# Optimization experiments

Measured on AMD Instinct MI355X. Metric: run time of the kernel, lower is better.

The kernel has to match this reference:

```python
import jax, jax.numpy as jnp
import numpy as np

N_NODES = 100000
N_EDGES = 1600000
IN_FEATS, HID, NUM_CLS = 128, 128, 40


def setup_inputs() -> dict:
    key = jax.random.key(0)
    ks = jax.random.split(key, 5)
    x = jax.random.normal(ks[0], (N_NODES, IN_FEATS), dtype=jnp.float32)
    # xavier-like scale for weights
    W1 = jax.random.normal(ks[1], (IN_FEATS, HID), dtype=jnp.float32) * (1.0 / np.sqrt(IN_FEATS))
    b1 = jnp.zeros((HID,), dtype=jnp.float32)
    W2 = jax.random.normal(ks[2], (HID, NUM_CLS), dtype=jnp.float32) * (1.0 / np.sqrt(HID))
    b2 = jnp.zeros((NUM_CLS,), dtype=jnp.float32)
    src = jax.random.randint(ks[3], (N_EDGES,), 0, N_NODES, dtype=jnp.int32)
    dst = jax.random.randint(ks[4], (N_EDGES,), 0, N_NODES, dtype=jnp.int32)
    return {"x": x, "W1": W1, "b1": b1, "W2": W2, "b2": b2, "src": src, "dst": dst}


def _graph_conv(h, W, b, src, dst, src_norm, dst_norm, n_nodes):
    # DGL GraphConv, norm='both': D_out^{-1/2} A D_in^{-1/2} H W + b
    # (weight-first vs aggregate-first ordering in DGL is mathematically identical)
    hs = h * src_norm[:, None]                      # [N, d] source-side norm
    msg = hs[src]                                   # [E, d] gather
    agg = jax.ops.segment_sum(msg, dst, num_segments=n_nodes)  # [N, d] scatter-add
    agg = agg * dst_norm[:, None]                   # dest-side norm
    return agg @ W + b


def reference(x, W1, b1, W2, b2, src, dst):
    n = x.shape[0]
    ones = jnp.ones(src.shape[0], dtype=x.dtype)
    out_deg = jnp.clip(jax.ops.segment_sum(ones, src, num_segments=n), 1.0)
    in_deg = jnp.clip(jax.ops.segment_sum(ones, dst, num_segments=n), 1.0)
    src_norm = out_deg ** -0.5
    dst_norm = in_deg ** -0.5
    h = jax.nn.relu(_graph_conv(x, W1, b1, src, dst, src_norm, dst_norm, n))
    return _graph_conv(h, W2, b2, src, dst, src_norm, dst_norm, n)
```

## Files before the change

kernel.cpp:

```cpp
#include <hip/hip_runtime.h>

constexpr int NN   = 100000;
constexpr int NE   = 1600000;
constexpr int INF  = 128;
constexpr int NC   = 40;

constexpr int BKSH = 9;
constexpr int NBK  = (NN + 511) / 512;
constexpr int EPB  = 4096;
constexpr int PBLK = (NE + EPB - 1) / EPB;
constexpr int CAP  = 14336;
constexpr int HB   = 391;

typedef __attribute__((ext_vector_type(8))) short short8;
typedef __attribute__((ext_vector_type(4))) float f32x4;

__device__ __forceinline__ float bflo(unsigned int u) { return __uint_as_float(u << 16); }
__device__ __forceinline__ float bfhi(unsigned int u) { return __uint_as_float(u & 0xffff0000u); }
__device__ __forceinline__ unsigned short f2bf(float f) {
    unsigned int u = __float_as_uint(f);
    return (unsigned short)((u + 0x7fffu + ((u >> 16) & 1u)) >> 16);
}
__device__ __forceinline__ unsigned int pack2(float a, float b) {
    return (unsigned int)f2bf(a) | ((unsigned int)f2bf(b) << 16);
}

__global__ __launch_bounds__(256) void histconv_kernel(const int* __restrict__ src,
                                                       const int* __restrict__ dst,
                                                       unsigned int* __restrict__ bcntD,
                                                       unsigned int* __restrict__ bcntS,
                                                       const float* __restrict__ x,
                                                       const float* __restrict__ W1,
                                                       const float* __restrict__ W2,
                                                       unsigned short* __restrict__ xh,
                                                       unsigned short* __restrict__ w1t,
                                                       unsigned short* __restrict__ w2t) {
    const int b = blockIdx.x;
    const int tid = threadIdx.x;
    if (b < HB) {
        __shared__ unsigned int hcD[NBK];
        __shared__ unsigned int hcS[NBK];
        for (int i = tid; i < NBK; i += 256) { hcD[i] = 0u; hcS[i] = 0u; }
        __syncthreads();
        int gid = b * 256 + tid;
        int stride = HB * 256;
        for (int e = gid; e < NE; e += stride) {
            atomicAdd(&hcD[dst[e] >> BKSH], 1u);
            atomicAdd(&hcS[src[e] >> BKSH], 1u);
        }
        __syncthreads();
        for (int i = tid; i < NBK; i += 256) {
            if (hcD[i]) atomicAdd(&bcntD[i], hcD[i]);
            if (hcS[i]) atomicAdd(&bcntS[i], hcS[i]);
        }
    } else if (b < HB + 6250) {
        int j = (b - HB) * 256 + tid;
        float4 v0 = ((const float4*)x)[2 * j];
        float4 v1 = ((const float4*)x)[2 * j + 1];
        uint4 o;
        o.x = pack2(v0.x, v0.y);
        o.y = pack2(v0.z, v0.w);
        o.z = pack2(v1.x, v1.y);
        o.w = pack2(v1.z, v1.w);
        ((uint4*)xh)[j] = o;
    } else if (b == HB + 6250) {
        for (int i = tid; i < 128 * 128; i += 256) {
            int k = i >> 7, n = i & 127;
            w1t[n * 128 + k] = f2bf(W1[i]);
        }
    } else {
        for (int i = tid; i < 48 * 128; i += 256) {
            int n = i >> 7, k = i & 127;
            w2t[i] = f2bf((n < NC) ? W2[k * NC + n] : 0.f);
        }
    }
}

__global__ __launch_bounds__(256) void partition_kernel(const int* __restrict__ src,
                                                        const int* __restrict__ dst,
                                                        const unsigned int* __restrict__ bcntD,
                                                        const unsigned int* __restrict__ bcntS,
                                                        int* __restrict__ curD_g,
                                                        int* __restrict__ curS_g,
                                                        int* __restrict__ epartsD,
                                                        unsigned short* __restrict__ epartsS) {
    __shared__ int sc[256];
    __shared__ int cntD[NBK], gadjD[NBK], curD[NBK];
    __shared__ int cntS[NBK], gadjS[NBK], curS[NBK];
    __shared__ int baselD[NBK], baselS[NBK];
    __shared__ int stageD[EPB];
    __shared__ unsigned short stageS[EPB];
    __shared__ unsigned char bidD[EPB];
    __shared__ unsigned char bidS[EPB];
    const int tid = threadIdx.x;
    const int e0 = blockIdx.x * EPB;
    const int total = min(EPB, NE - e0);

    {
        int v = (tid < NBK) ? (int)bcntD[tid] : 0;
        sc[tid] = v;
        __syncthreads();
        for (int off = 1; off < 256; off <<= 1) {
            int t = (tid >= off) ? sc[tid - off] : 0;
            __syncthreads();
            sc[tid] += t;
            __syncthreads();
        }
        if (tid < NBK) baselD[tid] = sc[tid] - v;
        __syncthreads();
        v = (tid < NBK) ? (int)bcntS[tid] : 0;
        sc[tid] = v;
        __syncthreads();
        for (int off = 1; off < 256; off <<= 1) {
            int t = (tid >= off) ? sc[tid - off] : 0;
            __syncthreads();
            sc[tid] += t;
            __syncthreads();
        }
        if (tid < NBK) baselS[tid] = sc[tid] - v;
    }
    for (int i = tid; i < NBK; i += 256) { cntD[i] = 0; cntS[i] = 0; }
    __syncthreads();
    for (int i = tid; i < total; i += 256) {
        atomicAdd(&cntD[dst[e0 + i] >> BKSH], 1);
        atomicAdd(&cntS[src[e0 + i] >> BKSH], 1);
    }
    __syncthreads();
    {
        int v = (tid < NBK) ? cntD[tid] : 0;
        sc[tid] = v;
        __syncthreads();
        for (int off = 1; off < 256; off <<= 1) {
            int t = (tid >= off) ? sc[tid - off] : 0;
            __syncthreads();
            sc[tid] += t;
            __syncthreads();
        }
        if (tid < NBK) {
            int excl = sc[tid] - v;
            curD[tid] = excl;
            int g = (v > 0) ? atomicAdd(&curD_g[tid], v) : 0;
            gadjD[tid] = baselD[tid] + g - excl;
        }
        __syncthreads();
        v = (tid < NBK) ? cntS[tid] : 0;
        sc[tid] = v;
        __syncthreads();
        for (int off = 1; off < 256; off <<= 1) {
            int t = (tid >= off) ? sc[tid - off] : 0;
            __syncthreads();
            sc[tid] += t;
            __syncthreads();
        }
        if (tid < NBK) {
            int excl = sc[tid] - v;
            curS[tid] = excl;
            int g = (v > 0) ? atomicAdd(&curS_g[tid], v) : 0;
            gadjS[tid] = baselS[tid] + g - excl;
        }
    }
    __syncthreads();
    for (int i = tid; i < total; i += 256) {
        int s = src[e0 + i];
        int d = dst[e0 + i];
        int bD = d >> BKSH;
        int offD = atomicAdd(&curD[bD], 1);
        stageD[offD] = s | ((d - (bD << BKSH)) << 17);
        bidD[offD] = (unsigned char)bD;
        int bS = s >> BKSH;
        int offS = atomicAdd(&curS[bS], 1);
        stageS[offS] = (unsigned short)(s - (bS << BKSH));
        bidS[offS] = (unsigned char)bS;
    }
    __syncthreads();
    for (int j = tid; j < total; j += 256) {
        int b = bidD[j];
        epartsD[gadjD[b] + j] = stageD[j];
    }
    for (int j = tid; j < total; j += 256) {
        int b = bidS[j];
        epartsS[gadjS[b] + j] = stageS[j];
    }
}

__global__ __launch_bounds__(512) void pass2_kernel(const int* __restrict__ epartsD,
                                                    const unsigned short* __restrict__ epartsS,
                                                    const unsigned int* __restrict__ bcntD,
                                                    const unsigned int* __restrict__ bcntS,
                                                    int* __restrict__ row_ptr,
                                                    int* __restrict__ esrc,
                                                    float* __restrict__ srcn,
                                                    float* __restrict__ dstn) {
    __shared__ int hist[512];
    __shared__ int cur[512];
    __shared__ int histS[512];
    __shared__ int lesrc[CAP];
    __shared__ int base_s, cnt_s, baseS_s, cntS_s;
    const int tid = threadIdx.x;
    const int b = blockIdx.x;

    {
        int v = (tid < NBK) ? (int)bcntD[tid] : 0;
        hist[tid] = v;
        __syncthreads();
        for (int off = 1; off < 512; off <<= 1) {
            int t = (tid >= off) ? hist[tid - off] : 0;
            __syncthreads();
            hist[tid] += t;
            __syncthreads();
        }
        if (tid == b) { base_s = hist[b] - v; cnt_s = v; }
        __syncthreads();
        v = (tid < NBK) ? (int)bcntS[tid] : 0;
        hist[tid] = v;
        __syncthreads();
        for (int off = 1; off < 512; off <<= 1) {
            int t = (tid >= off) ? hist[tid - off] : 0;
            __syncthreads();
            hist[tid] += t;
            __syncthreads();
        }
        if (tid == b) { baseS_s = hist[b] - v; cntS_s = v; }
        __syncthreads();
    }
    const int base = base_s;
    const int cnt = cnt_s;
    const int baseS = baseS_s;
    const int cntS = cntS_s;
    const int n0 = b << BKSH;
    const int nloc = min(512, NN - n0);

    hist[tid] = 0;
    histS[tid] = 0;
    __syncthreads();
    for (int j = tid; j < cnt; j += 512)
        atomicAdd(&hist[epartsD[base + j] >> 17], 1);
    for (int j = tid; j < cntS; j += 512)
        atomicAdd(&histS[(int)epartsS[baseS + j]], 1);
    __syncthreads();
    int myc = hist[tid];
    int mycS = histS[tid];
    for (int off = 1; off < 512; off <<= 1) {
        int t = (tid >= off) ? hist[tid - off] : 0;
        __syncthreads();
        hist[tid] += t;
        __syncthreads();
    }
    int excl = hist[tid] - myc;
    cur[tid] = excl;
    if (tid < nloc) {
        int g = n0 + tid;
        row_ptr[g] = base + excl;
        dstn[g] = rsqrtf(fmaxf((float)myc, 1.0f));
        srcn[g] = rsqrtf(fmaxf((float)mycS, 1.0f));
    }
    if (b == NBK - 1 && tid == 0) row_ptr[NN] = NE;
    __syncthreads();
    if (cnt <= CAP) {
        for (int j = tid; j < cnt; j += 512) {
            int rec = epartsD[base + j];
            int pos = atomicAdd(&cur[rec >> 17], 1);
            lesrc[pos] = rec & 0x1FFFF;
        }
        __syncthreads();
        for (int j = tid; j < cnt; j += 512) esrc[base + j] = lesrc[j];
    } else {
        for (int j = tid; j < cnt; j += 512) {
            int rec = epartsD[base + j];
            int pos = atomicAdd(&cur[rec >> 17], 1);
            esrc[base + pos] = rec & 0x1FFFF;
        }
    }
}

__global__ __launch_bounds__(256) void fused_kernel(const int* __restrict__ row_ptr,
                                                    const int* __restrict__ esrc,
                                                    const unsigned short* __restrict__ xh,
                                                    const float* __restrict__ srcn,
                                                    const unsigned short* __restrict__ w1t,
                                                    const unsigned short* __restrict__ w2t,
                                                    const float* __restrict__ b1,
                                                    const float* __restrict__ dstn,
                                                    unsigned short* __restrict__ hwb) {
    __shared__ unsigned short At[64 * 128];
    __shared__ float dn[64], sn[64], b1l[128];
    const int tid  = threadIdx.x;
    const int r0   = blockIdx.x * 64;
    const int wv   = tid >> 6;
    const int lane = tid & 63;

    if (tid < 64) {
        int r = r0 + tid;
        dn[tid] = (r < NN) ? dstn[r] : 0.f;
        sn[tid] = (r < NN) ? srcn[r] : 0.f;
    }
    if (tid >= 64 && tid < 192) b1l[tid - 64] = b1[tid - 64];
    __syncthreads();

    const int quad = lane >> 4;
    const int l16  = lane & 15;
    for (int i = 0; i < 16; ++i) {
        const int node = r0 + wv * 16 + i;
        float a0 = 0.f, a1 = 0.f, a2 = 0.f, a3 = 0.f;
        float a4 = 0.f, a5 = 0.f, a6 = 0.f, a7 = 0.f;
        if (node < NN) {
            int beg = __builtin_amdgcn_readfirstlane(row_ptr[node]);
            int end = __builtin_amdgcn_readfirstlane(row_ptr[node + 1]);
            for (int e = beg; e < end; e += 24) {
                const int rem = end - e;
                int s[6];
#pragma unroll
                for (int t = 0; t < 6; ++t) {
                    int slot = t * 4 + quad;
                    s[t] = esrc[(slot < rem) ? (e + slot) : beg];
                }
                float n[6];
                uint4 u[6];
#pragma unroll
                for (int t = 0; t < 6; ++t) {
                    int slot = t * 4 + quad;
                    n[t] = (slot < rem) ? srcn[s[t]] : 0.f;
                    u[t] = ((const uint4*)(xh + (size_t)s[t] * INF))[l16];
                }
#pragma unroll
                for (int t = 0; t < 6; ++t) {
                    a0 += bflo(u[t].x) * n[t];
                    a1 += bfhi(u[t].x) * n[t];
                    a2 += bflo(u[t].y) * n[t];
                    a3 += bfhi(u[t].y) * n[t];
                    a4 += bflo(u[t].z) * n[t];
                    a5 += bfhi(u[t].z) * n[t];
                    a6 += bflo(u[t].w) * n[t];
                    a7 += bfhi(u[t].w) * n[t];
                }
            }
        }
        a0 += __shfl_down(a0, 32); a1 += __shfl_down(a1, 32);
        a2 += __shfl_down(a2, 32); a3 += __shfl_down(a3, 32);
        a4 += __shfl_down(a4, 32); a5 += __shfl_down(a5, 32);
        a6 += __shfl_down(a6, 32); a7 += __shfl_down(a7, 32);
        a0 += __shfl_down(a0, 16); a1 += __shfl_down(a1, 16);
        a2 += __shfl_down(a2, 16); a3 += __shfl_down(a3, 16);
        a4 += __shfl_down(a4, 16); a5 += __shfl_down(a5, 16);
        a6 += __shfl_down(a6, 16); a7 += __shfl_down(a7, 16);
        if (lane < 16) {
            uint4 o;
            o.x = pack2(a0, a1);
            o.y = pack2(a2, a3);
            o.z = pack2(a4, a5);
            o.w = pack2(a6, a7);
            *(uint4*)&At[(wv * 16 + i) * 128 + l16 * 8] = o;
        }
    }

    const int lrow  = lane & 15;
    const int lquad = lane >> 4;

    short8 afrag[4];
#pragma unroll
    for (int ks = 0; ks < 4; ++ks)
        afrag[ks] = *(const short8*)&At[(wv * 16 + lrow) * 128 + ks * 32 + lquad * 8];
    float hreg[8][4];
#pragma unroll
    for (int nt = 0; nt < 8; ++nt) {
        f32x4 acc = {0.f, 0.f, 0.f, 0.f};
#pragma unroll
        for (int ks = 0; ks < 4; ++ks) {
            short8 bfr = *(const short8*)&w1t[(nt * 16 + lrow) * 128 + ks * 32 + lquad * 8];
            acc = __builtin_amdgcn_mfma_f32_16x16x32_bf16(afrag[ks], bfr, acc, 0, 0, 0);
        }
#pragma unroll
        for (int i = 0; i < 4; ++i) hreg[nt][i] = acc[i];
    }
#pragma unroll
    for (int nt = 0; nt < 8; ++nt) {
        int col = nt * 16 + lrow;
        float bb = b1l[col];
#pragma unroll
        for (int i = 0; i < 4; ++i) {
            int row = wv * 16 + lquad * 4 + i;
            At[row * 128 + col] = f2bf(fmaxf(hreg[nt][i] * dn[row] + bb, 0.f));
        }
    }

#pragma unroll
    for (int ks = 0; ks < 4; ++ks)
        afrag[ks] = *(const short8*)&At[(wv * 16 + lrow) * 128 + ks * 32 + lquad * 8];
#pragma unroll
    for (int nt = 0; nt < 3; ++nt) {
        f32x4 acc = {0.f, 0.f, 0.f, 0.f};
#pragma unroll
        for (int ks = 0; ks < 4; ++ks) {
            short8 bfr = *(const short8*)&w2t[(nt * 16 + lrow) * 128 + ks * 32 + lquad * 8];
            acc = __builtin_amdgcn_mfma_f32_16x16x32_bf16(afrag[ks], bfr, acc, 0, 0, 0);
        }
        int col = nt * 16 + lrow;
        if (col < NC) {
#pragma unroll
            for (int i = 0; i < 4; ++i) {
                int row = wv * 16 + lquad * 4 + i;
                int grow = r0 + row;
                if (grow < NN)
                    hwb[(size_t)grow * NC + col] = f2bf(acc[i] * sn[row]);
            }
        }
    }
}

__global__ __launch_bounds__(256) void gather2_kernel(const int* __restrict__ row_ptr,
                                                      const int* __restrict__ esrc,
                                                      const unsigned short* __restrict__ hwb,
                                                      const float* __restrict__ dst_norm,
                                                      const float* __restrict__ b2,
                                                      float* __restrict__ out) {
    int node = (blockIdx.x * blockDim.x + threadIdx.x) >> 6;
    int lane = threadIdx.x & 63;
    if (node >= NN) return;
    int beg = __builtin_amdgcn_readfirstlane(row_ptr[node]);
    int end = __builtin_amdgcn_readfirstlane(row_ptr[node + 1]);
    const int g = lane / 10;
    const int j = lane - g * 10;
    const bool active = (g < 6);
    float4 acc = make_float4(0.f, 0.f, 0.f, 0.f);
    for (int e = beg; e < end; e += 18) {
        const int rem = end - e;
        int s[3];
        float m[3];
#pragma unroll
        for (int q = 0; q < 3; ++q) {
            int slot = q * 6 + g;
            bool v = active && (slot < rem);
            int idx = v ? (e + slot) : beg;
            s[q] = esrc[idx];
            m[q] = v ? 1.f : 0.f;
        }
        uint2 u[3];
#pragma unroll
        for (int q = 0; q < 3; ++q)
            u[q] = ((const uint2*)(hwb + (size_t)s[q] * NC))[j];
#pragma unroll
        for (int q = 0; q < 3; ++q) {
            acc.x += bflo(u[q].x) * m[q];
            acc.y += bfhi(u[q].x) * m[q];
            acc.z += bflo(u[q].y) * m[q];
            acc.w += bfhi(u[q].y) * m[q];
        }
    }
    float4 tot = acc;
#pragma unroll
    for (int k = 1; k < 6; ++k) {
        tot.x += __shfl(acc.x, j + 10 * k);
        tot.y += __shfl(acc.y, j + 10 * k);
        tot.z += __shfl(acc.z, j + 10 * k);
        tot.w += __shfl(acc.w, j + 10 * k);
    }
    if (lane < 10) {
        float dnv = dst_norm[node];
        float4 bb = ((const float4*)b2)[j];
        float4 o;
        o.x = tot.x * dnv + bb.x;
        o.y = tot.y * dnv + bb.y;
        o.z = tot.z * dnv + bb.z;
        o.w = tot.w * dnv + bb.w;
        ((float4*)(out + (size_t)node * NC))[j] = o;
    }
}

extern "C" void kernel_launch(void* const* d_in, const int* in_sizes, int n_in,
                              void* d_out, int out_size, void* d_ws, size_t ws_size,
                              hipStream_t stream) {
    const float* x   = (const float*)d_in[0];
    const float* W1  = (const float*)d_in[1];
    const float* b1  = (const float*)d_in[2];
    const float* W2  = (const float*)d_in[3];
    const float* b2  = (const float*)d_in[4];
    const int*   src = (const int*)d_in[5];
    const int*   dst = (const int*)d_in[6];
    float* out = (float*)d_out;

    float* srcn = (float*)d_ws;
    unsigned int* bcntD = (unsigned int*)(srcn + NN);
    unsigned int* bcntS = bcntD + 256;
    int* curD = (int*)(bcntS + 256);
    int* curS = curD + 256;
    int* row_ptr = curS + 256;
    float* dstn  = (float*)(row_ptr + NN + 1);
    int* esrc    = (int*)(dstn + NN);
    size_t ofs = (size_t)NN + 1024 + (NN + 1) + NN + NE;
    ofs = (ofs + 3) & ~(size_t)3;
    unsigned short* xh   = (unsigned short*)((float*)d_ws + ofs);
    unsigned short* w1t  = xh + (size_t)NN * INF;
    unsigned short* w2t  = w1t + 128 * 128;
    unsigned short* hwb  = w2t + 48 * 128;

    int* epartsD = (int*)d_out;
    unsigned short* epartsS = (unsigned short*)(epartsD + NE);

    hipMemsetAsync(bcntD, 0, 1024 * sizeof(int), stream);

    histconv_kernel<<<HB + 6252, 256, 0, stream>>>(src, dst, bcntD, bcntS,
                                                   x, W1, W2, xh, w1t, w2t);
    partition_kernel<<<PBLK, 256, 0, stream>>>(src, dst, bcntD, bcntS, curD, curS,
                                               epartsD, epartsS);
    pass2_kernel<<<NBK, 512, 0, stream>>>(epartsD, epartsS, bcntD, bcntS,
                                          row_ptr, esrc, srcn, dstn);
    fused_kernel<<<(NN + 63) / 64, 256, 0, stream>>>(row_ptr, esrc, xh, srcn,
                                                     w1t, w2t, b1, dstn, hwb);
    gather2_kernel<<<(NN * 64 + 255) / 256, 256, 0, stream>>>(row_ptr, esrc, hwb,
                                                              dstn, b2, out);
}
```

Baseline: 318.7 us.

## Replace two-pass bucket partition CSR build with global-atomic degree count and scatter

Replaces the shared-memory bucketed two-pass partition (partition_kernel plus pass2_kernel) with direct global atomic per-node in/out degree counting in the histogram kernel, a per-bucket scan kernel that writes row_ptr and cursors, and a simple scatter kernel using global atomics on per-node cursors. This cuts the staging traffic through the output buffer and the extra passes over the edge list. In exchange it adds 3.2M random global atomics for degrees and 1.6M contended atomic cursor updates with scattered writes, and edge order within each row becomes nondeterministic, which can change floating-point summation order.

```diff
diff --git a/kernel.cpp b/kernel.cpp
--- a/kernel.cpp
+++ b/kernel.cpp
@@ -7,9 +7,6 @@
 
 constexpr int BKSH = 9;
 constexpr int NBK  = (NN + 511) / 512;
-constexpr int EPB  = 4096;
-constexpr int PBLK = (NE + EPB - 1) / EPB;
-constexpr int CAP  = 14336;
 constexpr int HB   = 391;
 
 typedef __attribute__((ext_vector_type(8))) short short8;
@@ -27,8 +24,9 @@
 
 __global__ __launch_bounds__(256) void histconv_kernel(const int* __restrict__ src,
                                                        const int* __restrict__ dst,
+                                                       int* __restrict__ indeg,
+                                                       int* __restrict__ outdeg,
                                                        unsigned int* __restrict__ bcntD,
-                                                       unsigned int* __restrict__ bcntS,
                                                        const float* __restrict__ x,
                                                        const float* __restrict__ W1,
                                                        const float* __restrict__ W2,
@@ -39,20 +37,20 @@
     const int tid = threadIdx.x;
     if (b < HB) {
         __shared__ unsigned int hcD[NBK];
-        __shared__ unsigned int hcS[NBK];
-        for (int i = tid; i < NBK; i += 256) { hcD[i] = 0u; hcS[i] = 0u; }
+        for (int i = tid; i < NBK; i += 256) hcD[i] = 0u;
         __syncthreads();
         int gid = b * 256 + tid;
         int stride = HB * 256;
         for (int e = gid; e < NE; e += stride) {
-            atomicAdd(&hcD[dst[e] >> BKSH], 1u);
-            atomicAdd(&hcS[src[e] >> BKSH], 1u);
-        }
-        __syncthreads();
-        for (int i = tid; i < NBK; i += 256) {
+            int d = dst[e];
+            int s = src[e];
+            atomicAdd(&indeg[d], 1);
+            atomicAdd(&outdeg[s], 1);
+            atomicAdd(&hcD[d >> BKSH], 1u);
+        }
+        __syncthreads();
+        for (int i = tid; i < NBK; i += 256)
             if (hcD[i]) atomicAdd(&bcntD[i], hcD[i]);
-            if (hcS[i]) atomicAdd(&bcntS[i], hcS[i]);
-        }
     } else if (b < HB + 6250) {
         int j = (b - HB) * 256 + tid;
         float4 v0 = ((const float4*)x)[2 * j];
@@ -76,201 +74,69 @@
     }
 }
 
-__global__ __launch_bounds__(256) void partition_kernel(const int* __restrict__ src,
-                                                        const int* __restrict__ dst,
-                                                        const unsigned int* __restrict__ bcntD,
-                                                        const unsigned int* __restrict__ bcntS,
-                                                        int* __restrict__ curD_g,
-                                                        int* __restrict__ curS_g,
-                                                        int* __restrict__ epartsD,
-                                                        unsigned short* __restrict__ epartsS) {
-    __shared__ int sc[256];
-    __shared__ int cntD[NBK], gadjD[NBK], curD[NBK];
-    __shared__ int cntS[NBK], gadjS[NBK], curS[NBK];
-    __shared__ int baselD[NBK], baselS[NBK];
-    __shared__ int stageD[EPB];
-    __shared__ unsigned short stageS[EPB];
-    __shared__ unsigned char bidD[EPB];
-    __shared__ unsigned char bidS[EPB];
+__global__ __launch_bounds__(512) void scan_kernel(const unsigned int* __restrict__ bcntD,
+                                                   const int* __restrict__ indeg,
+                                                   const int* __restrict__ outdeg,
+                                                   int* __restrict__ row_ptr,
+                                                   int* __restrict__ cur,
+                                                   float* __restrict__ dstn,
+                                                   float* __restrict__ srcn) {
+    __shared__ int sc[512];
+    __shared__ int base_s;
     const int tid = threadIdx.x;
-    const int e0 = blockIdx.x * EPB;
-    const int total = min(EPB, NE - e0);
+    const int b = blockIdx.x;
 
     {
         int v = (tid < NBK) ? (int)bcntD[tid] : 0;
         sc[tid] = v;
         __syncthreads();
-        for (int off = 1; off < 256; off <<= 1) {
+        for (int off = 1; off < 512; off <<= 1) {
             int t = (tid >= off) ? sc[tid - off] : 0;
             __syncthreads();
             sc[tid] += t;
             __syncthreads();
         }
-        if (tid < NBK) baselD[tid] = sc[tid] - v;
-        __syncthreads();
-        v = (tid < NBK) ? (int)bcntS[tid] : 0;
-        sc[tid] = v;
-        __syncthreads();
-        for (int off = 1; off < 256; off <<= 1) {
-            int t = (tid >= off) ? sc[tid - off] : 0;
-            __syncthreads();
-            sc[tid] += t;
-            __syncthreads();
-        }
-        if (tid < NBK) baselS[tid] = sc[tid] - v;
-    }
-    for (int i = tid; i < NBK; i += 256) { cntD[i] = 0; cntS[i] = 0; }
-    __syncthreads();
-    for (int i = tid; i < total; i += 256) {
-        atomicAdd(&cntD[dst[e0 + i] >> BKSH], 1);
-        atomicAdd(&cntS[src[e0 + i] >> BKSH], 1);
-    }
-    __syncthreads();
-    {
-        int v = (tid < NBK) ? cntD[tid] : 0;
-        sc[tid] = v;
-        __syncthreads();
-        for (int off = 1; off < 256; off <<= 1) {
-            int t = (tid >= off) ? sc[tid - off] : 0;
-            __syncthreads();
-            sc[tid] += t;
-            __syncthreads();
-        }
-        if (tid < NBK) {
-            int excl = sc[tid] - v;
-            curD[tid] = excl;
-            int g = (v > 0) ? atomicAdd(&curD_g[tid], v) : 0;
-            gadjD[tid] = baselD[tid] + g - excl;
-        }
-        __syncthreads();
-        v = (tid < NBK) ? cntS[tid] : 0;
-        sc[tid] = v;
-        __syncthreads();
-        for (int off = 1; off < 256; off <<= 1) {
-            int t = (tid >= off) ? sc[tid - off] : 0;
-            __syncthreads();
-            sc[tid] += t;
-            __syncthreads();
-        }
-        if (tid < NBK) {
-            int excl = sc[tid] - v;
-            curS[tid] = excl;
-            int g = (v > 0) ? atomicAdd(&curS_g[tid], v) : 0;
-            gadjS[tid] = baselS[tid] + g - excl;
-        }
-    }
-    __syncthreads();
-    for (int i = tid; i < total; i += 256) {
-        int s = src[e0 + i];
-        int d = dst[e0 + i];
-        int bD = d >> BKSH;
-        int offD = atomicAdd(&curD[bD], 1);
-        stageD[offD] = s | ((d - (bD << BKSH)) << 17);
-        bidD[offD] = (unsigned char)bD;
-        int bS = s >> BKSH;
-        int offS = atomicAdd(&curS[bS], 1);
-        stageS[offS] = (unsigned short)(s - (bS << BKSH));
-        bidS[offS] = (unsigned char)bS;
-    }
-    __syncthreads();
-    for (int j = tid; j < total; j += 256) {
-        int b = bidD[j];
-        epartsD[gadjD[b] + j] = stageD[j];
-    }
-    for (int j = tid; j < total; j += 256) {
-        int b = bidS[j];
-        epartsS[gadjS[b] + j] = stageS[j];
-    }
-}
-
-__global__ __launch_bounds__(512) void pass2_kernel(const int* __restrict__ epartsD,
-                                                    const unsigned short* __restrict__ epartsS,
-                                                    const unsigned int* __restrict__ bcntD,
-                                                    const unsigned int* __restrict__ bcntS,
-                                                    int* __restrict__ row_ptr,
-                                                    int* __restrict__ esrc,
-                                                    float* __restrict__ srcn,
-                                                    float* __restrict__ dstn) {
-    __shared__ int hist[512];
-    __shared__ int cur[512];
-    __shared__ int histS[512];
-    __shared__ int lesrc[CAP];
-    __shared__ int base_s, cnt_s, baseS_s, cntS_s;
-    const int tid = threadIdx.x;
-    const int b = blockIdx.x;
-
-    {
-        int v = (tid < NBK) ? (int)bcntD[tid] : 0;
-        hist[tid] = v;
-        __syncthreads();
-        for (int off = 1; off < 512; off <<= 1) {
-            int t = (tid >= off) ? hist[tid - off] : 0;
-            __syncthreads();
-            hist[tid] += t;
-            __syncthreads();
-        }
-        if (tid == b) { base_s = hist[b] - v; cnt_s = v; }
-        __syncthreads();
-        v = (tid < NBK) ? (int)bcntS[tid] : 0;
-        hist[tid] = v;
-        __syncthreads();
-        for (int off = 1; off < 512; off <<= 1) {
-            int t = (tid >= off) ? hist[tid - off] : 0;
-            __syncthreads();
-            hist[tid] += t;
-            __syncthreads();
-        }
-        if (tid == b) { baseS_s = hist[b] - v; cntS_s = v; }
+        if (tid == b) base_s = sc[b] - v;
         __syncthreads();
     }
     const int base = base_s;
-    const int cnt = cnt_s;
-    const int baseS = baseS_s;
-    const int cntS = cntS_s;
     const int n0 = b << BKSH;
     const int nloc = min(512, NN - n0);
 
-    hist[tid] = 0;
-    histS[tid] = 0;
+    int deg = 0, odeg = 0;
+    if (tid < nloc) {
+        deg = indeg[n0 + tid];
+        odeg = outdeg[n0 + tid];
+    }
+    sc[tid] = deg;
     __syncthreads();
-    for (int j = tid; j < cnt; j += 512)
-        atomicAdd(&hist[epartsD[base + j] >> 17], 1);
-    for (int j = tid; j < cntS; j += 512)
-        atomicAdd(&histS[(int)epartsS[baseS + j]], 1);
-    __syncthreads();
-    int myc = hist[tid];
-    int mycS = histS[tid];
     for (int off = 1; off < 512; off <<= 1) {
-        int t = (tid >= off) ? hist[tid - off] : 0;
-        __syncthreads();
-        hist[tid] += t;
-        __syncthreads();
-    }
-    int excl = hist[tid] - myc;
-    cur[tid] = excl;
+        int t = (tid >= off) ? sc[tid - off] : 0;
+        __syncthreads();
+        sc[tid] += t;
+        __syncthreads();
+    }
     if (tid < nloc) {
         int g = n0 + tid;
+        int excl = sc[tid] - deg;
         row_ptr[g] = base + excl;
-        dstn[g] = rsqrtf(fmaxf((float)myc, 1.0f));
-        srcn[g] = rsqrtf(fmaxf((float)mycS, 1.0f));
+        cur[g] = base + excl;
+        dstn[g] = rsqrtf(fmaxf((float)deg, 1.0f));
+        srcn[g] = rsqrtf(fmaxf((float)odeg, 1.0f));
     }
     if (b == NBK - 1 && tid == 0) row_ptr[NN] = NE;
-    __syncthreads();
-    if (cnt <= CAP) {
-        for (int j = tid; j < cnt; j += 512) {
-            int rec = epartsD[base + j];
-            int pos = atomicAdd(&cur[rec >> 17], 1);
-            lesrc[pos] = rec & 0x1FFFF;
-        }
-        __syncthreads();
-        for (int j = tid; j < cnt; j += 512) esrc[base + j] = lesrc[j];
-    } else {
-        for (int j = tid; j < cnt; j += 512) {
-            int rec = epartsD[base + j];
-            int pos = atomicAdd(&cur[rec >> 17], 1);
-            esrc[base + pos] = rec & 0x1FFFF;
-        }
-    }
+}
+
+__global__ __launch_bounds__(256) void scatter_kernel(const int* __restrict__ src,
+                                                      const int* __restrict__ dst,
+                                                      int* __restrict__ cur,
+                                                      int* __restrict__ esrc) {
+    int e = blockIdx.x * 256 + threadIdx.x;
+    if (e >= NE) return;
+    int d = dst[e];
+    int s = src[e];
+    int pos = atomicAdd(&cur[d], 1);
+    esrc[pos] = s;
 }
 
 __global__ __launch_bounds__(256) void fused_kernel(const int* __restrict__ row_ptr,
@@ -478,32 +344,28 @@
     const int*   dst = (const int*)d_in[6];
     float* out = (float*)d_out;
 
-    float* srcn = (float*)d_ws;
-    unsigned int* bcntD = (unsigned int*)(srcn + NN);
-    unsigned int* bcntS = bcntD + 256;
-    int* curD = (int*)(bcntS + 256);
-    int* curS = curD + 256;
-    int* row_ptr = curS + 256;
-    float* dstn  = (float*)(row_ptr + NN + 1);
-    int* esrc    = (int*)(dstn + NN);
-    size_t ofs = (size_t)NN + 1024 + (NN + 1) + NN + NE;
+    int* indeg  = (int*)d_ws;
+    int* outdeg = indeg + NN;
+    unsigned int* bcntD = (unsigned int*)(outdeg + NN);
+    int* row_ptr = (int*)(bcntD + 256);
+    int* cur     = row_ptr + NN + 1;
+    float* dstn  = (float*)(cur + NN);
+    float* srcn  = dstn + NN;
+    int* esrc    = (int*)(srcn + NN);
+    size_t ofs = (size_t)(2 * NN + 256) + (NN + 1) + 3 * (size_t)NN + NE;
     ofs = (ofs + 3) & ~(size_t)3;
     unsigned short* xh   = (unsigned short*)((float*)d_ws + ofs);
     unsigned short* w1t  = xh + (size_t)NN * INF;
     unsigned short* w2t  = w1t + 128 * 128;
     unsigned short* hwb  = w2t + 48 * 128;
 
-    int* epartsD = (int*)d_out;
-    unsigned short* epartsS = (unsigned short*)(epartsD + NE);
-
-    hipMemsetAsync(bcntD, 0, 1024 * sizeof(int), stream);
-
-    histconv_kernel<<<HB + 6252, 256, 0, stream>>>(src, dst, bcntD, bcntS,
+    hipMemsetAsync(indeg, 0, (size_t)(2 * NN + 256) * sizeof(int), stream);
+
+    histconv_kernel<<<HB + 6252, 256, 0, stream>>>(src, dst, indeg, outdeg, bcntD,
                                                    x, W1, W2, xh, w1t, w2t);
-    partition_kernel<<<PBLK, 256, 0, stream>>>(src, dst, bcntD, bcntS, curD, curS,
-                                               epartsD, epartsS);
-    pass2_kernel<<<NBK, 512, 0, stream>>>(epartsD, epartsS, bcntD, bcntS,
-                                          row_ptr, esrc, srcn, dstn);
+    scan_kernel<<<NBK, 512, 0, stream>>>(bcntD, indeg, outdeg,
+                                         row_ptr, cur, dstn, srcn);
+    scatter_kernel<<<(NE + 255) / 256, 256, 0, stream>>>(src, dst, cur, esrc);
     fused_kernel<<<(NN + 63) / 64, 256, 0, stream>>>(row_ptr, esrc, xh, srcn,
                                                      w1t, w2t, b1, dstn, hwb);
     gather2_kernel<<<(NN * 64 + 255) / 256, 256, 0, stream>>>(row_ptr, esrc, hwb,
```

Result: slower. 502.6 us (+57.7%).

## Hoist bucket base scan into one kernel and interleave two-node gathers

Applied to the files above, without the earlier changes.

A new single-block kernel computes the exclusive scans of the bucket counts once, so the partition and pass2 blocks no longer each redo both scans with many barriers. In the fused layer-1 kernel, each wave now aggregates two destination nodes at a time, with row pointers loaded once per wave and shared by shuffles. This doubles the number of independent gather loads in flight to hide memory latency, and occupancy is pinned with launch_bounds(256,4). The cost is more registers per thread, wasted slots when the two nodes' degrees differ, and one extra tiny kernel launch.

```diff
diff --git a/kernel.cpp b/kernel.cpp
--- a/kernel.cpp
+++ b/kernel.cpp
@@ -76,10 +76,39 @@
     }
 }
 
+__global__ __launch_bounds__(256) void basescan_kernel(const unsigned int* __restrict__ bcntD,
+                                                       const unsigned int* __restrict__ bcntS,
+                                                       int* __restrict__ baseD,
+                                                       int* __restrict__ baseS) {
+    __shared__ int sc[256];
+    const int tid = threadIdx.x;
+    int v = (tid < NBK) ? (int)bcntD[tid] : 0;
+    sc[tid] = v;
+    __syncthreads();
+    for (int off = 1; off < 256; off <<= 1) {
+        int t = (tid >= off) ? sc[tid - off] : 0;
+        __syncthreads();
+        sc[tid] += t;
+        __syncthreads();
+    }
+    if (tid < NBK) baseD[tid] = sc[tid] - v;
+    __syncthreads();
+    v = (tid < NBK) ? (int)bcntS[tid] : 0;
+    sc[tid] = v;
+    __syncthreads();
+    for (int off = 1; off < 256; off <<= 1) {
+        int t = (tid >= off) ? sc[tid - off] : 0;
+        __syncthreads();
+        sc[tid] += t;
+        __syncthreads();
+    }
+    if (tid < NBK) baseS[tid] = sc[tid] - v;
+}
+
 __global__ __launch_bounds__(256) void partition_kernel(const int* __restrict__ src,
                                                         const int* __restrict__ dst,
-                                                        const unsigned int* __restrict__ bcntD,
-                                                        const unsigned int* __restrict__ bcntS,
+                                                        const int* __restrict__ baseD,
+                                                        const int* __restrict__ baseS,
                                                         int* __restrict__ curD_g,
                                                         int* __restrict__ curS_g,
                                                         int* __restrict__ epartsD,
@@ -87,7 +116,6 @@
     __shared__ int sc[256];
     __shared__ int cntD[NBK], gadjD[NBK], curD[NBK];
     __shared__ int cntS[NBK], gadjS[NBK], curS[NBK];
-    __shared__ int baselD[NBK], baselS[NBK];
     __shared__ int stageD[EPB];
     __shared__ unsigned short stageS[EPB];
     __shared__ unsigned char bidD[EPB];
@@ -96,8 +124,15 @@
     const int e0 = blockIdx.x * EPB;
     const int total = min(EPB, NE - e0);
 
+    for (int i = tid; i < NBK; i += 256) { cntD[i] = 0; cntS[i] = 0; }
+    __syncthreads();
+    for (int i = tid; i < total; i += 256) {
+        atomicAdd(&cntD[dst[e0 + i] >> BKSH], 1);
+        atomicAdd(&cntS[src[e0 + i] >> BKSH], 1);
+    }
+    __syncthreads();
     {
-        int v = (tid < NBK) ? (int)bcntD[tid] : 0;
+        int v = (tid < NBK) ? cntD[tid] : 0;
         sc[tid] = v;
         __syncthreads();
         for (int off = 1; off < 256; off <<= 1) {
@@ -106,9 +141,14 @@
             sc[tid] += t;
             __syncthreads();
         }
-        if (tid < NBK) baselD[tid] = sc[tid] - v;
-        __syncthreads();
-        v = (tid < NBK) ? (int)bcntS[tid] : 0;
+        if (tid < NBK) {
+            int excl = sc[tid] - v;
+            curD[tid] = excl;
+            int g = (v > 0) ? atomicAdd(&curD_g[tid], v) : 0;
+            gadjD[tid] = baseD[tid] + g - excl;
+        }
+        __syncthreads();
+        v = (tid < NBK) ? cntS[tid] : 0;
         sc[tid] = v;
         __syncthreads();
         for (int off = 1; off < 256; off <<= 1) {
@@ -117,46 +157,11 @@
             sc[tid] += t;
             __syncthreads();
         }
-        if (tid < NBK) baselS[tid] = sc[tid] - v;
-    }
-    for (int i = tid; i < NBK; i += 256) { cntD[i] = 0; cntS[i] = 0; }
-    __syncthreads();
-    for (int i = tid; i < total; i += 256) {
-        atomicAdd(&cntD[dst[e0 + i] >> BKSH], 1);
-        atomicAdd(&cntS[src[e0 + i] >> BKSH], 1);
-    }
-    __syncthreads();
-    {
-        int v = (tid < NBK) ? cntD[tid] : 0;
-        sc[tid] = v;
-        __syncthreads();
-        for (int off = 1; off < 256; off <<= 1) {
-            int t = (tid >= off) ? sc[tid - off] : 0;
-            __syncthreads();
-            sc[tid] += t;
-            __syncthreads();
-        }
-        if (tid < NBK) {
-            int excl = sc[tid] - v;
-            curD[tid] = excl;
-            int g = (v > 0) ? atomicAdd(&curD_g[tid], v) : 0;
-            gadjD[tid] = baselD[tid] + g - excl;
-        }
-        __syncthreads();
-        v = (tid < NBK) ? cntS[tid] : 0;
-        sc[tid] = v;
-        __syncthreads();
-        for (int off = 1; off < 256; off <<= 1) {
-            int t = (tid >= off) ? sc[tid - off] : 0;
-            __syncthreads();
-            sc[tid] += t;
-            __syncthreads();
-        }
         if (tid < NBK) {
             int excl = sc[tid] - v;
             curS[tid] = excl;
             int g = (v > 0) ? atomicAdd(&curS_g[tid], v) : 0;
-            gadjS[tid] = baselS[tid] + g - excl;
+            gadjS[tid] = baseS[tid] + g - excl;
         }
     }
     __syncthreads();
@@ -185,6 +190,8 @@
 
 __global__ __launch_bounds__(512) void pass2_kernel(const int* __restrict__ epartsD,
                                                     const unsigned short* __restrict__ epartsS,
+                                                    const int* __restrict__ baseD,
+                                                    const int* __restrict__ baseS_g,
                                                     const unsigned int* __restrict__ bcntD,
                                                     const unsigned int* __restrict__ bcntS,
                                                     int* __restrict__ row_ptr,
@@ -195,38 +202,13 @@
     __shared__ int cur[512];
     __shared__ int histS[512];
     __shared__ int lesrc[CAP];
-    __shared__ int base_s, cnt_s, baseS_s, cntS_s;
     const int tid = threadIdx.x;
     const int b = blockIdx.x;
 
-    {
-        int v = (tid < NBK) ? (int)bcntD[tid] : 0;
-        hist[tid] = v;
-        __syncthreads();
-        for (int off = 1; off < 512; off <<= 1) {
-            int t = (tid >= off) ? hist[tid - off] : 0;
-            __syncthreads();
-            hist[tid] += t;
-            __syncthreads();
-        }
-        if (tid == b) { base_s = hist[b] - v; cnt_s = v; }
-        __syncthreads();
-        v = (tid < NBK) ? (int)bcntS[tid] : 0;
-        hist[tid] = v;
-        __syncthreads();
-        for (int off = 1; off < 512; off <<= 1) {
-            int t = (tid >= off) ? hist[tid - off] : 0;
-            __syncthreads();
-            hist[tid] += t;
-            __syncthreads();
-        }
-        if (tid == b) { baseS_s = hist[b] - v; cntS_s = v; }
-        __syncthreads();
-    }
-    const int base = base_s;
-    const int cnt = cnt_s;
-    const int baseS = baseS_s;
-    const int cntS = cntS_s;
+    const int base  = baseD[b];
+    const int cnt   = (int)bcntD[b];
+    const int baseS = baseS_g[b];
+    const int cntS  = (int)bcntS[b];
     const int n0 = b << BKSH;
     const int nloc = min(512, NN - n0);
 
@@ -273,15 +255,15 @@
     }
 }
 
-__global__ __launch_bounds__(256) void fused_kernel(const int* __restrict__ row_ptr,
-                                                    const int* __restrict__ esrc,
-                                                    const unsigned short* __restrict__ xh,
-                                                    const float* __restrict__ srcn,
-                                                    const unsigned short* __restrict__ w1t,
-                                                    const unsigned short* __restrict__ w2t,
-                                                    const float* __restrict__ b1,
-                                                    const float* __restrict__ dstn,
-                                                    unsigned short* __restrict__ hwb) {
+__global__ __launch_bounds__(256, 4) void fused_kernel(const int* __restrict__ row_ptr,
+                                                       const int* __restrict__ esrc,
+                                                       const unsigned short* __restrict__ xh,
+                                                       const float* __restrict__ srcn,
+                                                       const unsigned short* __restrict__ w1t,
+                                                       const unsigned short* __restrict__ w2t,
+                                                       const float* __restrict__ b1,
+                                                       const float* __restrict__ dstn,
+                                                       unsigned short* __restrict__ hwb) {
     __shared__ unsigned short At[64 * 128];
     __shared__ float dn[64], sn[64], b1l[128];
     const int tid  = threadIdx.x;
@@ -299,57 +281,74 @@
 
     const int quad = lane >> 4;
     const int l16  = lane & 15;
-    for (int i = 0; i < 16; ++i) {
-        const int node = r0 + wv * 16 + i;
-        float a0 = 0.f, a1 = 0.f, a2 = 0.f, a3 = 0.f;
-        float a4 = 0.f, a5 = 0.f, a6 = 0.f, a7 = 0.f;
-        if (node < NN) {
-            int beg = __builtin_amdgcn_readfirstlane(row_ptr[node]);
-            int end = __builtin_amdgcn_readfirstlane(row_ptr[node + 1]);
-            for (int e = beg; e < end; e += 24) {
-                const int rem = end - e;
-                int s[6];
-#pragma unroll
-                for (int t = 0; t < 6; ++t) {
-                    int slot = t * 4 + quad;
-                    s[t] = esrc[(slot < rem) ? (e + slot) : beg];
-                }
-                float n[6];
-                uint4 u[6];
-#pragma unroll
-                for (int t = 0; t < 6; ++t) {
-                    int slot = t * 4 + quad;
-                    n[t] = (slot < rem) ? srcn[s[t]] : 0.f;
-                    u[t] = ((const uint4*)(xh + (size_t)s[t] * INF))[l16];
-                }
-#pragma unroll
-                for (int t = 0; t < 6; ++t) {
-                    a0 += bflo(u[t].x) * n[t];
-                    a1 += bfhi(u[t].x) * n[t];
-                    a2 += bflo(u[t].y) * n[t];
-                    a3 += bfhi(u[t].y) * n[t];
-                    a4 += bflo(u[t].z) * n[t];
-                    a5 += bfhi(u[t].z) * n[t];
-                    a6 += bflo(u[t].w) * n[t];
-                    a7 += bfhi(u[t].w) * n[t];
-                }
+    const int n0w  = r0 + wv * 16;
+    const int rpv = row_ptr[min(n0w + min(lane, 16), NN)];
+
+    for (int p = 0; p < 8; ++p) {
+        const int begA = __shfl(rpv, 2 * p);
+        const int endA = __shfl(rpv, 2 * p + 1);
+        const int begB = endA;
+        const int endB = __shfl(rpv, 2 * p + 2);
+        float aA0 = 0.f, aA1 = 0.f, aA2 = 0.f, aA3 = 0.f;
+        float aA4 = 0.f, aA5 = 0.f, aA6 = 0.f, aA7 = 0.f;
+        float aB0 = 0.f, aB1 = 0.f, aB2 = 0.f, aB3 = 0.f;
+        float aB4 = 0.f, aB5 = 0.f, aB6 = 0.f, aB7 = 0.f;
+        for (int eA = begA, eB = begB; eA < endA || eB < endB; eA += 24, eB += 24) {
+            const int remA = endA - eA;
+            const int remB = endB - eB;
+            int sA[6], sB[6];
+#pragma unroll
+            for (int t = 0; t < 6; ++t) {
+                int slot = t * 4 + quad;
+                sA[t] = esrc[(slot < remA) ? (eA + slot) : 0];
+                sB[t] = esrc[(slot < remB) ? (eB + slot) : 0];
             }
-        }
-        a0 += __shfl_down(a0, 32); a1 += __shfl_down(a1, 32);
-        a2 += __shfl_down(a2, 32); a3 += __shfl_down(a3, 32);
-        a4 += __shfl_down(a4, 32); a5 += __shfl_down(a5, 32);
-        a6 += __shfl_down(a6, 32); a7 += __shfl_down(a7, 32);
-        a0 += __shfl_down(a0, 16); a1 += __shfl_down(a1, 16);
-        a2 += __shfl_down(a2, 16); a3 += __shfl_down(a3, 16);
-        a4 += __shfl_down(a4, 16); a5 += __shfl_down(a5, 16);
-        a6 += __shfl_down(a6, 16); a7 += __shfl_down(a7, 16);
+            float nA[6], nB[6];
+            uint4 uA[6], uB[6];
+#pragma unroll
+            for (int t = 0; t < 6; ++t) {
+                int slot = t * 4 + quad;
+                nA[t] = (slot < remA) ? srcn[sA[t]] : 0.f;
+                nB[t] = (slot < remB) ? srcn[sB[t]] : 0.f;
+                uA[t] = ((const uint4*)(xh + (size_t)sA[t] * INF))[l16];
+                uB[t] = ((const uint4*)(xh + (size_t)sB[t] * INF))[l16];
+            }
+#pragma unroll
+            for (int t = 0; t < 6; ++t) {
+                aA0 += bflo(uA[t].x) * nA[t]; aA1 += bfhi(uA[t].x) * nA[t];
+                aA2 += bflo(uA[t].y) * nA[t]; aA3 += bfhi(uA[t].y) * nA[t];
+                aA4 += bflo(uA[t].z) * nA[t]; aA5 += bfhi(uA[t].z) * nA[t];
+                aA6 += bflo(uA[t].w) * nA[t]; aA7 += bfhi(uA[t].w) * nA[t];
+                aB0 += bflo(uB[t].x) * nB[t]; aB1 += bfhi(uB[t].x) * nB[t];
+                aB2 += bflo(uB[t].y) * nB[t]; aB3 += bfhi(uB[t].y) * nB[t];
+                aB4 += bflo(uB[t].z) * nB[t]; aB5 += bfhi(uB[t].z) * nB[t];
+                aB6 += bflo(uB[t].w) * nB[t]; aB7 += bfhi(uB[t].w) * nB[t];
+            }
+        }
+        aA0 += __shfl_down(aA0, 32); aA1 += __shfl_down(aA1, 32);
+        aA2 += __shfl_down(aA2, 32); aA3 += __shfl_down(aA3, 32);
+        aA4 += __shfl_down(aA4, 32); aA5 += __shfl_down(aA5, 32);
+        aA6 += __shfl_down(aA6, 32); aA7 += __shfl_down(aA7, 32);
+        aB0 += __shfl_down(aB0, 32); aB1 += __shfl_down(aB1, 32);
+        aB2 += __shfl_down(aB2, 32); aB3 += __shfl_down(aB3, 32);
+        aB4 += __shfl_down(aB4, 32); aB5 += __shfl_down(aB5, 32);
+        aB6 += __shfl_down(aB6, 32); aB7 += __shfl_down(aB7, 32);
+        aA0 += __shfl_down(aA0, 16); aA1 += __shfl_down(aA1, 16);
+        aA2 += __shfl_down(aA2, 16); aA3 += __shfl_down(aA3, 16);
+        aA4 += __shfl_down(aA4, 16); aA5 += __shfl_down(aA5, 16);
+        aA6 += __shfl_down(aA6, 16); aA7 += __shfl_down(aA7, 16);
+        aB0 += __shfl_down(aB0, 16); aB1 += __shfl_down(aB1, 16);
+        aB2 += __shfl_down(aB2, 16); aB3 += __shfl_down(aB3, 16);
+        aB4 += __shfl_down(aB4, 16); aB5 += __shfl_down(aB5, 16);
+        aB6 += __shfl_down(aB6, 16); aB7 += __shfl_down(aB7, 16);
         if (lane < 16) {
-            uint4 o;
-            o.x = pack2(a0, a1);
-            o.y = pack2(a2, a3);
-            o.z = pack2(a4, a5);
-            o.w = pack2(a6, a7);
-            *(uint4*)&At[(wv * 16 + i) * 128 + l16 * 8] = o;
+            uint4 oA, oB;
+            oA.x = pack2(aA0, aA1); oA.y = pack2(aA2, aA3);
+            oA.z = pack2(aA4, aA5); oA.w = pack2(aA6, aA7);
+            oB.x = pack2(aB0, aB1); oB.y = pack2(aB2, aB3);
+            oB.z = pack2(aB4, aB5); oB.w = pack2(aB6, aB7);
+            *(uint4*)&At[(wv * 16 + 2 * p) * 128 + l16 * 8] = oA;
+            *(uint4*)&At[(wv * 16 + 2 * p + 1) * 128 + l16 * 8] = oB;
         }
     }
 
@@ -481,12 +480,14 @@
     float* srcn = (float*)d_ws;
     unsigned int* bcntD = (unsigned int*)(srcn + NN);
     unsigned int* bcntS = bcntD + 256;
-    int* curD = (int*)(bcntS + 256);
-    int* curS = curD + 256;
-    int* row_ptr = curS + 256;
+    int* curD  = (int*)(bcntS + 256);
+    int* curS  = curD + 256;
+    int* baseD = curS + 256;
+    int* baseS = baseD + 256;
+    int* row_ptr = baseS + 256;
     float* dstn  = (float*)(row_ptr + NN + 1);
     int* esrc    = (int*)(dstn + NN);
-    size_t ofs = (size_t)NN + 1024 + (NN + 1) + NN + NE;
+    size_t ofs = (size_t)NN + 1536 + (NN + 1) + NN + NE;
     ofs = (ofs + 3) & ~(size_t)3;
     unsigned short* xh   = (unsigned short*)((float*)d_ws + ofs);
     unsigned short* w1t  = xh + (size_t)NN * INF;
@@ -500,10 +501,11 @@
 
     histconv_kernel<<<HB + 6252, 256, 0, stream>>>(src, dst, bcntD, bcntS,
                                                    x, W1, W2, xh, w1t, w2t);
-    partition_kernel<<<PBLK, 256, 0, stream>>>(src, dst, bcntD, bcntS, curD, curS,
+    basescan_kernel<<<1, 256, 0, stream>>>(bcntD, bcntS, baseD, baseS);
+    partition_kernel<<<PBLK, 256, 0, stream>>>(src, dst, baseD, baseS, curD, curS,
                                                epartsD, epartsS);
-    pass2_kernel<<<NBK, 512, 0, stream>>>(epartsD, epartsS, bcntD, bcntS,
-                                          row_ptr, esrc, srcn, dstn);
+    pass2_kernel<<<NBK, 512, 0, stream>>>(epartsD, epartsS, baseD, baseS,
+                                          bcntD, bcntS, row_ptr, esrc, srcn, dstn);
     fused_kernel<<<(NN + 63) / 64, 256, 0, stream>>>(row_ptr, esrc, xh, srcn,
                                                      w1t, w2t, b1, dstn, hwb);
     gather2_kernel<<<(NN * 64 + 255) / 256, 256, 0, stream>>>(row_ptr, esrc, hwb,
```

Measured after the change: 307.7 us. 3.5% less time.
